# Kernel optimization log

Hardware: AMD Instinct MI355X
Metric: run time of the kernel (lower is better)

The kernel has to match this reference:

```python
import math
import jax, jax.numpy as jnp
import numpy as np

IN_D = 16
H_DIM = 256
NB_STEPS = 50
B = 8192


def _cc_weights(nb_steps):
    # Clenshaw-Curtis quadrature weights and nodes, exactly as the torch code.
    k = np.arange(0, nb_steps + 1, dtype=np.float64).reshape(-1, 1)
    lam = np.cos(k @ k.T * math.pi / nb_steps)
    lam[:, 0] = 0.5
    lam[:, -1] = 0.5 * lam[:, -1]
    lam = lam * 2.0 / nb_steps
    W = np.arange(0, nb_steps + 1, dtype=np.float64).reshape(-1, 1)
    W[1::2] = 0.0
    W = 2.0 / (1.0 - W ** 2)
    W[0] = 1.0
    W[1::2] = 0.0
    cc = (lam.T @ W).astype(np.float32)  # [nb_steps+1, 1]
    steps = np.cos(np.arange(0, nb_steps + 1) * math.pi / nb_steps).astype(np.float32)  # [nb_steps+1]
    return jnp.asarray(cc), jnp.asarray(steps)


def setup_inputs() -> dict:
    key = jax.random.key(0)
    ks = jax.random.split(key, 16)
    s = 0.05
    return {
        "x": jax.random.normal(ks[0], (B, 1), jnp.float32),
        "h": jax.random.normal(ks[1], (B, IN_D - 1), jnp.float32),
        "iw1": jax.random.normal(ks[2], (H_DIM, IN_D), jnp.float32) * s,
        "ib1": jax.random.normal(ks[3], (H_DIM,), jnp.float32) * s,
        "iw2": jax.random.normal(ks[4], (H_DIM, H_DIM), jnp.float32) * s,
        "ib2": jax.random.normal(ks[5], (H_DIM,), jnp.float32) * s,
        "iw3": jax.random.normal(ks[6], (1, H_DIM), jnp.float32) * s,
        "ib3": jax.random.normal(ks[7], (1,), jnp.float32) * s,
        "nw1": jax.random.normal(ks[8], (H_DIM, IN_D - 1), jnp.float32) * s,
        "nb1": jax.random.normal(ks[9], (H_DIM,), jnp.float32) * s,
        "nw2": jax.random.normal(ks[10], (H_DIM, H_DIM), jnp.float32) * s,
        "nb2": jax.random.normal(ks[11], (H_DIM,), jnp.float32) * s,
        "nw3": jax.random.normal(ks[12], (2, H_DIM), jnp.float32) * s,
        "nb3": jax.random.normal(ks[13], (2,), jnp.float32) * s,
        "nb_steps": NB_STEPS,
    }


def _integrand(z, iw1, ib1, iw2, ib2, iw3, ib3):
    # IntegrandNN: Linear-ReLU-Linear-ReLU-Linear-ELU, then +1.0
    a = jax.nn.relu(z @ iw1.T + ib1)
    a = jax.nn.relu(a @ iw2.T + ib2)
    return jax.nn.elu(a @ iw3.T + ib3) + 1.0


def reference(x, h, iw1, ib1, iw2, ib2, iw3, ib3, nw1, nb1, nw2, nb2, nw3, nb3, nb_steps):
    cc, steps = _cc_weights(int(nb_steps))  # cc: [N+1,1], steps: [N+1]
    Bn, n_pts = x.shape[0], int(nb_steps) + 1
    # x0 = 0, so quadrature nodes X_k = x * (steps_k + 1) / 2 -> [B, N+1, 1]
    X = x[:, None, :] * ((steps[None, :, None] + 1.0) * 0.5)
    Xf = X.reshape(-1, 1)                                             # [B*(N+1), 1]
    Hf = jnp.broadcast_to(h[:, None, :], (Bn, n_pts, h.shape[1])).reshape(-1, h.shape[1])
    z = jnp.concatenate([Xf, Hf], axis=1)                             # [B*(N+1), in_d]
    f = _integrand(z, iw1, ib1, iw2, ib2, iw3, ib3).reshape(Bn, n_pts, 1)
    integral = jnp.sum(f * cc[None, :, :], axis=1) * x * 0.5          # [B, 1]
    # conditioner net on h: Linear-ReLU-Linear-ReLU-Linear -> [B, 2]
    a = jax.nn.relu(h @ nw1.T + nb1)
    a = jax.nn.relu(a @ nw2.T + nb2)
    out = a @ nw3.T + nb3
    offset = out[:, :1]
    scaling = jnp.exp(out[:, 1:2])
    return scaling * integral + offset
```

## Files before the change

### kernel.cpp

```cpp
#include <hip/hip_runtime.h>
#include <hip/hip_bf16.h>
#include <math.h>

#define BATCH 8192
#define HD    256
#define NPTS  51
#define MTOT  (BATCH*NPTS)

typedef __bf16 bf16x8 __attribute__((ext_vector_type(8)));
typedef float  f32x4  __attribute__((ext_vector_type(4)));

#define OFF_IW2P  0
#define OFF_W1X   131072
#define OFF_CC    132096
#define OFF_STEPS 132352
#define OFF_OFFS  132608
#define OFF_SCAL  165376
#define OFF_G1    198144
#define OFF_FV0   8586752
#define OFF_FV1   10257920

__device__ __forceinline__ unsigned short f2bf(float f) {
    union { float f; unsigned u; } v; v.f = f;
    unsigned r = v.u + 0x7FFFu + ((v.u >> 16) & 1u);
    return (unsigned short)(r >> 16);
}

__device__ __forceinline__ unsigned pk2bf(float lo, float hi) {
    __hip_bfloat162 t = __float22bfloat162_rn(float2{lo, hi});
    union { __hip_bfloat162 b; unsigned u; } v; v.b = t;
    return v.u;
}

__global__ void k1_fused(const float* __restrict__ iw2, const float* __restrict__ nw1,
                         const float* __restrict__ iw1, const float* __restrict__ ib1,
                         const float* __restrict__ nb1, const float* __restrict__ h,
                         const float* __restrict__ nw2, const float* __restrict__ nb2,
                         const float* __restrict__ nw3, const float* __restrict__ nb3,
                         unsigned short* iw2p, float* w1xs, float* cc, float* steps,
                         float* __restrict__ g1, float* __restrict__ offs,
                         float* __restrict__ scal) {
    int blk = blockIdx.x, tid = threadIdx.x;
    if (blk < 256) {
        int t = blk * 256 + tid;
        int n = t >> 8, k = t & 255;
        int half = n >> 7, nl = n & 127, c = k >> 3, j = k & 7;
        iw2p[half * 32768 + c * 1024 + nl * 8 + j] = f2bf(iw2[t]);
    } else if (blk == 256) {
        w1xs[tid] = iw1[tid * 16];
        const float PI_F = 3.14159265358979323846f;
        if (tid <= 50) {
            int j = tid;
            float s = 0.f;
            for (int i = 0; i <= 50; i += 2) {
                float w = (i == 0) ? 1.f : 2.f / (1.f - (float)(i * i));
                float l;
                if (j == 0 || j == 50) l = 0.5f;
                else { int r = (i * j) % 100; l = __cosf((float)r * (PI_F / 50.f)); }
                s += l * w;
            }
            cc[j]    = s * (2.f / 50.f);
            steps[j] = __cosf((float)j * (PI_F / 50.f));
        }
    } else {
        __shared__ float hs[16][15];
        __shared__ unsigned short a1s[16][264];
        __shared__ float Pp[4 * 2 * 16];
        int b0 = (blk - 257) * 16, n = tid;
        if (tid < 240) { int bb = tid / 15, j = tid % 15; hs[bb][j] = h[(b0 + bb) * 15 + j]; }
        __syncthreads();
        float ir[16], nr[15];
        const float4* ip = (const float4*)(iw1 + n * 16);
        ((float4*)ir)[0] = ip[0]; ((float4*)ir)[1] = ip[1];
        ((float4*)ir)[2] = ip[2]; ((float4*)ir)[3] = ip[3];
        #pragma unroll
        for (int j = 0; j < 15; ++j) nr[j] = nw1[n * 15 + j];
        float bi = ib1[n], bn = nb1[n];
        #pragma unroll
        for (int bb = 0; bb < 16; ++bb) {
            float g = bi, a = bn;
            #pragma unroll
            for (int j = 0; j < 15; ++j) { float hv = hs[bb][j]; g += hv * ir[j + 1]; a += hv * nr[j]; }
            g1[(b0 + bb) * 256 + n] = g;
            a1s[bb][n] = f2bf(fmaxf(a, 0.f));
        }
        __syncthreads();

        int lane = tid & 63, w = tid >> 6, l16 = lane & 15, quad = lane >> 4;
        f32x4 acc[4];
        #pragma unroll
        for (int nt = 0; nt < 4; ++nt) acc[nt] = (f32x4){0.f, 0.f, 0.f, 0.f};
        #pragma unroll
        for (int ks = 0; ks < 8; ++ks) {
            bf16x8 af = *(const bf16x8*)&a1s[l16][ks * 32 + quad * 8];
            #pragma unroll
            for (int nt = 0; nt < 4; ++nt) {
                const float* np = nw2 + (w * 64 + nt * 16 + l16) * 256 + ks * 32 + quad * 8;
                float4 f0 = ((const float4*)np)[0];
                float4 f1 = ((const float4*)np)[1];
                union { uint4 u; bf16x8 v; } bf;
                bf.u.x = pk2bf(f0.x, f0.y); bf.u.y = pk2bf(f0.z, f0.w);
                bf.u.z = pk2bf(f1.x, f1.y); bf.u.w = pk2bf(f1.z, f1.w);
                acc[nt] = __builtin_amdgcn_mfma_f32_16x16x32_bf16(af, bf.v, acc[nt], 0, 0, 0);
            }
        }
        float p0[4], p1[4];
        #pragma unroll
        for (int i = 0; i < 4; ++i) { p0[i] = 0.f; p1[i] = 0.f; }
        #pragma unroll
        for (int nt = 0; nt < 4; ++nt) {
            int nn = w * 64 + nt * 16 + l16;
            float bias = nb2[nn], wa = nw3[nn], wb = nw3[256 + nn];
            #pragma unroll
            for (int i = 0; i < 4; ++i) {
                float v = acc[nt][i] + bias;
                v = v > 0.f ? v : 0.f;
                p0[i] += v * wa;
                p1[i] += v * wb;
            }
        }
        #pragma unroll
        for (int mask = 1; mask < 16; mask <<= 1)
            #pragma unroll
            for (int i = 0; i < 4; ++i) {
                p0[i] += __shfl_xor(p0[i], mask, 64);
                p1[i] += __shfl_xor(p1[i], mask, 64);
            }
        if (l16 == 0) {
            #pragma unroll
            for (int i = 0; i < 4; ++i) {
                int r = quad * 4 + i;
                Pp[w * 32 + r]      = p0[i];
                Pp[w * 32 + 16 + r] = p1[i];
            }
        }
        __syncthreads();
        if (tid < 16) {
            float s0 = Pp[tid]      + Pp[32 + tid] + Pp[64 + tid] + Pp[96 + tid]  + nb3[0];
            float s1 = Pp[16 + tid] + Pp[48 + tid] + Pp[80 + tid] + Pp[112 + tid] + nb3[1];
            offs[b0 + tid] = s0;
            scal[b0 + tid] = __expf(s1);
        }
    }
}

__launch_bounds__(256, 4)
__global__ void k2_main(const float* __restrict__ x, const float* __restrict__ g1,
                        const float* __restrict__ w1xs, const unsigned short* __restrict__ iw2p,
                        const float* __restrict__ ib2, const float* __restrict__ iw3,
                        const float* __restrict__ steps,
                        float* __restrict__ fv0, float* __restrict__ fv1) {
    __shared__ __align__(16) unsigned char smem[37888];
    float* Pp = (float*)smem;

    int tid = threadIdx.x;
    int bid = blockIdx.x;
    int hf  = bid & 1;
    int m0  = (bid >> 1) * 128;
    int lane = tid & 63, w = tid >> 6;
    int l16 = lane & 15, quad = lane >> 4;

    unsigned blo = (unsigned)(((unsigned long long)(unsigned)m0 * 657931ull) >> 25);

    const unsigned char* bsrc = (const unsigned char*)iw2p + hf * 65536 + tid * 16;

    #pragma unroll
    for (int it = 0; it < 4; ++it)
        __builtin_amdgcn_global_load_lds(
            (const __attribute__((address_space(1))) unsigned int*)(bsrc + it * 4096),
            (__attribute__((address_space(3))) unsigned int*)(smem + tid * 16 + it * 4096),
            16, 0, 0);
    __builtin_amdgcn_global_load_lds(
        (const __attribute__((address_space(1))) unsigned int*)((const unsigned char*)(g1 + blo * 256) + tid * 16),
        (__attribute__((address_space(3))) unsigned int*)(smem + 32768 + tid * 16),
        16, 0, 0);
    if (w == 0)
        __builtin_amdgcn_global_load_lds(
            (const __attribute__((address_space(1))) unsigned int*)((const unsigned char*)w1xs + lane * 16),
            (__attribute__((address_space(3))) unsigned int*)(smem + 36864 + lane * 16),
            16, 0, 0);

    float xs_[2]; int rel_[2];
    #pragma unroll
    for (int mt = 0; mt < 2; ++mt) {
        int m = m0 + w * 32 + mt * 16 + l16;
        unsigned b = (unsigned)(((unsigned long long)(unsigned)m * 657931ull) >> 25);
        int p = m - (int)b * 51;
        xs_[mt] = x[b] * (steps[p] + 1.f) * 0.5f;
        rel_[mt] = (int)(b - blo) * 256;
    }

    f32x4 acc[2][8];
    #pragma unroll
    for (int mt = 0; mt < 2; ++mt)
        #pragma unroll
        for (int nt = 0; nt < 8; ++nt)
            acc[mt][nt] = (f32x4){0.f, 0.f, 0.f, 0.f};

    const float* Ag = (const float*)(smem + 32768);
    const float* Wl = (const float*)(smem + 36864);

    #pragma unroll
    for (int kc = 0; kc < 4; ++kc) {
        __syncthreads();
        if (kc < 3) {
            const unsigned char* s2 = bsrc + (kc + 1) * 16384;
            unsigned char* d2 = smem + ((kc + 1) & 1) * 16384 + tid * 16;
            #pragma unroll
            for (int it = 0; it < 4; ++it)
                __builtin_amdgcn_global_load_lds(
                    (const __attribute__((address_space(1))) unsigned int*)(s2 + it * 4096),
                    (__attribute__((address_space(3))) unsigned int*)(d2 + it * 4096),
                    16, 0, 0);
        }
        const unsigned short* Bl = (const unsigned short*)(smem + (kc & 1) * 16384);
        #pragma unroll
        for (int s = 0; s < 2; ++s) {
            int ks = kc * 2 + s;
            int ko = ks * 32 + quad * 8;
            int cl = s * 4 + quad;

            union { uint4 u; bf16x8 v; } af[2];
            {
                float4 w0 = ((const float4*)(Wl + ko))[0];
                float4 w1 = ((const float4*)(Wl + ko))[1];
                #pragma unroll
                for (int mt = 0; mt < 2; ++mt) {
                    const float* gp = Ag + rel_[mt] + ko;
                    float4 ga  = ((const float4*)gp)[0];
                    float4 gb2 = ((const float4*)gp)[1];
                    float xs = xs_[mt];
                    float a0 = fmaxf(ga.x  + xs * w0.x, 0.f);
                    float a1 = fmaxf(ga.y  + xs * w0.y, 0.f);
                    float a2 = fmaxf(ga.z  + xs * w0.z, 0.f);
                    float a3 = fmaxf(ga.w  + xs * w0.w, 0.f);
                    float a4 = fmaxf(gb2.x + xs * w1.x, 0.f);
                    float a5 = fmaxf(gb2.y + xs * w1.y, 0.f);
                    float a6 = fmaxf(gb2.z + xs * w1.z, 0.f);
                    float a7 = fmaxf(gb2.w + xs * w1.w, 0.f);
                    af[mt].u.x = pk2bf(a0, a1); af[mt].u.y = pk2bf(a2, a3);
                    af[mt].u.z = pk2bf(a4, a5); af[mt].u.w = pk2bf(a6, a7);
                }
            }

            #pragma unroll
            for (int g = 0; g < 2; ++g) {
                bf16x8 bfr[4];
                #pragma unroll
                for (int nt = 0; nt < 4; ++nt)
                    bfr[nt] = *(const bf16x8*)(Bl + (cl * 128 + (g * 4 + nt) * 16 + l16) * 8);
                #pragma unroll
                for (int mt = 0; mt < 2; ++mt)
                    #pragma unroll
                    for (int nt = 0; nt < 4; ++nt)
                        acc[mt][g * 4 + nt] = __builtin_amdgcn_mfma_f32_16x16x32_bf16(
                            af[mt].v, bfr[nt], acc[mt][g * 4 + nt], 0, 0, 0);
            }
        }
    }

    float pf[2][4];
    #pragma unroll
    for (int mt = 0; mt < 2; ++mt)
        #pragma unroll
        for (int i = 0; i < 4; ++i) pf[mt][i] = 0.f;
    #pragma unroll
    for (int nt = 0; nt < 8; ++nt) {
        int n = hf * 128 + nt * 16 + l16;
        float bias = ib2[n], w3 = iw3[n];
        #pragma unroll
        for (int mt = 0; mt < 2; ++mt)
            #pragma unroll
            for (int i = 0; i < 4; ++i) {
                float v = acc[mt][nt][i] + bias;
                v = v > 0.f ? v : 0.f;
                pf[mt][i] += v * w3;
            }
    }
    __syncthreads();
    #pragma unroll
    for (int mt = 0; mt < 2; ++mt)
        #pragma unroll
        for (int i = 0; i < 4; ++i) {
            int row = w * 32 + mt * 16 + quad * 4 + i;
            Pp[row * 20 + l16] = pf[mt][i];
        }
    __syncthreads();
    if (tid < 128) {
        const float4* pp = (const float4*)(Pp + tid * 20);
        float4 v0 = pp[0], v1 = pp[1], v2 = pp[2], v3 = pp[3];
        float s = v0.x + v0.y + v0.z + v0.w + v1.x + v1.y + v1.z + v1.w
                + v2.x + v2.y + v2.z + v2.w + v3.x + v3.y + v3.z + v3.w;
        (hf ? fv1 : fv0)[m0 + tid] = s;
    }
}

__global__ void k4_final(const float* __restrict__ x, const float* __restrict__ fv0,
                         const float* __restrict__ fv1, const float* __restrict__ ib3,
                         const float* __restrict__ cc,
                         const float* __restrict__ offs, const float* __restrict__ scal,
                         float* __restrict__ out) {
    int tid = threadIdx.x;
    int wv = tid >> 6, lane = tid & 63;
    int b = blockIdx.x * 4 + wv;
    float v = 0.f;
    if (lane < 51) {
        int m = b * 51 + lane;
        float s = fv0[m] + fv1[m] + ib3[0];
        float f = s > 0.f ? s + 1.f : __expf(s);
        v = f * cc[lane];
    }
    #pragma unroll
    for (int mask = 1; mask < 64; mask <<= 1) v += __shfl_xor(v, mask, 64);
    if (lane == 0)
        out[b] = scal[b] * (0.5f * x[b] * v) + offs[b];
}

extern "C" void kernel_launch(void* const* d_in, const int* in_sizes, int n_in,
                              void* d_out, int out_size, void* d_ws, size_t ws_size,
                              hipStream_t stream) {
    const float* x   = (const float*)d_in[0];
    const float* h   = (const float*)d_in[1];
    const float* iw1 = (const float*)d_in[2];
    const float* ib1 = (const float*)d_in[3];
    const float* iw2 = (const float*)d_in[4];
    const float* ib2 = (const float*)d_in[5];
    const float* iw3 = (const float*)d_in[6];
    const float* ib3 = (const float*)d_in[7];
    const float* nw1 = (const float*)d_in[8];
    const float* nb1 = (const float*)d_in[9];
    const float* nw2 = (const float*)d_in[10];
    const float* nb2 = (const float*)d_in[11];
    const float* nw3 = (const float*)d_in[12];
    const float* nb3 = (const float*)d_in[13];
    float* out = (float*)d_out;

    char* ws = (char*)d_ws;
    unsigned short* iw2p = (unsigned short*)(ws + OFF_IW2P);
    float* w1xs  = (float*)(ws + OFF_W1X);
    float* cc    = (float*)(ws + OFF_CC);
    float* steps = (float*)(ws + OFF_STEPS);
    float* offs  = (float*)(ws + OFF_OFFS);
    float* scal  = (float*)(ws + OFF_SCAL);
    float* g1    = (float*)(ws + OFF_G1);
    float* fv0   = (float*)(ws + OFF_FV0);
    float* fv1   = (float*)(ws + OFF_FV1);

    k1_fused<<<dim3(769), dim3(256), 0, stream>>>(iw2, nw1, iw1, ib1, nb1, h,
                                                  nw2, nb2, nw3, nb3,
                                                  iw2p, w1xs, cc, steps, g1, offs, scal);
    k2_main<<<dim3((MTOT / 128) * 2), dim3(256), 0, stream>>>(x, g1, w1xs, iw2p, ib2, iw3,
                                                              steps, fv0, fv1);
    k4_final<<<dim3(BATCH / 4), dim3(256), 0, stream>>>(x, fv0, fv1, ib3, cc, offs, scal, out);
}
```

Measured before the change: 162.8 us.

## Compute full N=256 per block in k2, fuse ELU and CC weighting into epilogue

Each k2 block now covers all 256 output columns instead of splitting N across two blocks. This halves the block count and removes the duplicated first-layer activation computation and the second partial-sum buffer. The layer-1 precompute g1 and the w1x weights are read straight from global memory instead of staged in LDS, and ELU plus the quadrature-weight multiply move into the k2 epilogue so k4 only reduces. In exchange the accumulator doubles to 32 MFMA tiles and LDS grows to 64KB, which lowers the occupancy bound from 4 to 2 blocks per CU.

```diff
diff --git a/kernel.cpp b/kernel.cpp
--- a/kernel.cpp
+++ b/kernel.cpp
@@ -3,7 +3,6 @@
 #include <math.h>
 
 #define BATCH 8192
-#define HD    256
 #define NPTS  51
 #define MTOT  (BATCH*NPTS)
 
@@ -17,8 +16,7 @@
 #define OFF_OFFS  132608
 #define OFF_SCAL  165376
 #define OFF_G1    198144
-#define OFF_FV0   8586752
-#define OFF_FV1   10257920
+#define OFF_FVALS 8586752
 
 __device__ __forceinline__ unsigned short f2bf(float f) {
     union { float f; unsigned u; } v; v.f = f;
@@ -144,40 +142,29 @@
     }
 }
 
-__launch_bounds__(256, 4)
+__launch_bounds__(256, 2)
 __global__ void k2_main(const float* __restrict__ x, const float* __restrict__ g1,
                         const float* __restrict__ w1xs, const unsigned short* __restrict__ iw2p,
                         const float* __restrict__ ib2, const float* __restrict__ iw3,
-                        const float* __restrict__ steps,
-                        float* __restrict__ fv0, float* __restrict__ fv1) {
-    __shared__ __align__(16) unsigned char smem[37888];
+                        const float* __restrict__ ib3, const float* __restrict__ cc,
+                        const float* __restrict__ steps, float* __restrict__ fvals) {
+    __shared__ __align__(16) unsigned char smem[65536];
     float* Pp = (float*)smem;
 
     int tid = threadIdx.x;
-    int bid = blockIdx.x;
-    int hf  = bid & 1;
-    int m0  = (bid >> 1) * 128;
+    int m0  = blockIdx.x * 128;
     int lane = tid & 63, w = tid >> 6;
     int l16 = lane & 15, quad = lane >> 4;
 
-    unsigned blo = (unsigned)(((unsigned long long)(unsigned)m0 * 657931ull) >> 25);
-
-    const unsigned char* bsrc = (const unsigned char*)iw2p + hf * 65536 + tid * 16;
-
-    #pragma unroll
-    for (int it = 0; it < 4; ++it)
+    int hh = tid >> 7, t7 = tid & 127;
+    const unsigned char* bsrc = (const unsigned char*)iw2p + hh * 65536 + t7 * 16;
+    unsigned char* bds0 = smem + hh * 16384 + t7 * 16;
+
+    #pragma unroll
+    for (int it = 0; it < 8; ++it)
         __builtin_amdgcn_global_load_lds(
-            (const __attribute__((address_space(1))) unsigned int*)(bsrc + it * 4096),
-            (__attribute__((address_space(3))) unsigned int*)(smem + tid * 16 + it * 4096),
-            16, 0, 0);
-    __builtin_amdgcn_global_load_lds(
-        (const __attribute__((address_space(1))) unsigned int*)((const unsigned char*)(g1 + blo * 256) + tid * 16),
-        (__attribute__((address_space(3))) unsigned int*)(smem + 32768 + tid * 16),
-        16, 0, 0);
-    if (w == 0)
-        __builtin_amdgcn_global_load_lds(
-            (const __attribute__((address_space(1))) unsigned int*)((const unsigned char*)w1xs + lane * 16),
-            (__attribute__((address_space(3))) unsigned int*)(smem + 36864 + lane * 16),
+            (const __attribute__((address_space(1))) unsigned int*)(bsrc + it * 2048),
+            (__attribute__((address_space(3))) unsigned int*)(bds0 + it * 2048),
             16, 0, 0);
 
     float xs_[2]; int rel_[2];
@@ -187,68 +174,66 @@
         unsigned b = (unsigned)(((unsigned long long)(unsigned)m * 657931ull) >> 25);
         int p = m - (int)b * 51;
         xs_[mt] = x[b] * (steps[p] + 1.f) * 0.5f;
-        rel_[mt] = (int)(b - blo) * 256;
-    }
-
-    f32x4 acc[2][8];
+        rel_[mt] = (int)b * 256;
+    }
+
+    f32x4 acc[2][16];
     #pragma unroll
     for (int mt = 0; mt < 2; ++mt)
         #pragma unroll
-        for (int nt = 0; nt < 8; ++nt)
+        for (int nt = 0; nt < 16; ++nt)
             acc[mt][nt] = (f32x4){0.f, 0.f, 0.f, 0.f};
-
-    const float* Ag = (const float*)(smem + 32768);
-    const float* Wl = (const float*)(smem + 36864);
 
     #pragma unroll
     for (int kc = 0; kc < 4; ++kc) {
         __syncthreads();
         if (kc < 3) {
             const unsigned char* s2 = bsrc + (kc + 1) * 16384;
-            unsigned char* d2 = smem + ((kc + 1) & 1) * 16384 + tid * 16;
-            #pragma unroll
-            for (int it = 0; it < 4; ++it)
+            unsigned char* d2 = smem + ((kc + 1) & 1) * 32768 + hh * 16384 + t7 * 16;
+            #pragma unroll
+            for (int it = 0; it < 8; ++it)
                 __builtin_amdgcn_global_load_lds(
-                    (const __attribute__((address_space(1))) unsigned int*)(s2 + it * 4096),
-                    (__attribute__((address_space(3))) unsigned int*)(d2 + it * 4096),
+                    (const __attribute__((address_space(1))) unsigned int*)(s2 + it * 2048),
+                    (__attribute__((address_space(3))) unsigned int*)(d2 + it * 2048),
                     16, 0, 0);
         }
-        const unsigned short* Bl = (const unsigned short*)(smem + (kc & 1) * 16384);
+        const unsigned short* Bl = (const unsigned short*)(smem + (kc & 1) * 32768);
         #pragma unroll
         for (int s = 0; s < 2; ++s) {
-            int ks = kc * 2 + s;
-            int ko = ks * 32 + quad * 8;
+            int ko = kc * 64 + s * 32 + quad * 8;
             int cl = s * 4 + quad;
 
+            float4 w0 = ((const float4*)(w1xs + ko))[0];
+            float4 w1 = ((const float4*)(w1xs + ko))[1];
+
             union { uint4 u; bf16x8 v; } af[2];
-            {
-                float4 w0 = ((const float4*)(Wl + ko))[0];
-                float4 w1 = ((const float4*)(Wl + ko))[1];
-                #pragma unroll
-                for (int mt = 0; mt < 2; ++mt) {
-                    const float* gp = Ag + rel_[mt] + ko;
-                    float4 ga  = ((const float4*)gp)[0];
-                    float4 gb2 = ((const float4*)gp)[1];
-                    float xs = xs_[mt];
-                    float a0 = fmaxf(ga.x  + xs * w0.x, 0.f);
-                    float a1 = fmaxf(ga.y  + xs * w0.y, 0.f);
-                    float a2 = fmaxf(ga.z  + xs * w0.z, 0.f);
-                    float a3 = fmaxf(ga.w  + xs * w0.w, 0.f);
-                    float a4 = fmaxf(gb2.x + xs * w1.x, 0.f);
-                    float a5 = fmaxf(gb2.y + xs * w1.y, 0.f);
-                    float a6 = fmaxf(gb2.z + xs * w1.z, 0.f);
-                    float a7 = fmaxf(gb2.w + xs * w1.w, 0.f);
-                    af[mt].u.x = pk2bf(a0, a1); af[mt].u.y = pk2bf(a2, a3);
-                    af[mt].u.z = pk2bf(a4, a5); af[mt].u.w = pk2bf(a6, a7);
-                }
-            }
-
-            #pragma unroll
-            for (int g = 0; g < 2; ++g) {
+            #pragma unroll
+            for (int mt = 0; mt < 2; ++mt) {
+                const float* gp = g1 + rel_[mt] + ko;
+                float4 ga  = ((const float4*)gp)[0];
+                float4 gb2 = ((const float4*)gp)[1];
+                float xs = xs_[mt];
+                float a0 = fmaxf(fmaf(xs, w0.x, ga.x),  0.f);
+                float a1 = fmaxf(fmaf(xs, w0.y, ga.y),  0.f);
+                float a2 = fmaxf(fmaf(xs, w0.z, ga.z),  0.f);
+                float a3 = fmaxf(fmaf(xs, w0.w, ga.w),  0.f);
+                float a4 = fmaxf(fmaf(xs, w1.x, gb2.x), 0.f);
+                float a5 = fmaxf(fmaf(xs, w1.y, gb2.y), 0.f);
+                float a6 = fmaxf(fmaf(xs, w1.z, gb2.z), 0.f);
+                float a7 = fmaxf(fmaf(xs, w1.w, gb2.w), 0.f);
+                af[mt].u.x = pk2bf(a0, a1); af[mt].u.y = pk2bf(a2, a3);
+                af[mt].u.z = pk2bf(a4, a5); af[mt].u.w = pk2bf(a6, a7);
+            }
+
+            #pragma unroll
+            for (int g = 0; g < 4; ++g) {
                 bf16x8 bfr[4];
                 #pragma unroll
-                for (int nt = 0; nt < 4; ++nt)
-                    bfr[nt] = *(const bf16x8*)(Bl + (cl * 128 + (g * 4 + nt) * 16 + l16) * 8);
+                for (int nt = 0; nt < 4; ++nt) {
+                    int n = (g * 4 + nt) * 16 + l16;
+                    int h2 = n >> 7, nl = n & 127;
+                    bfr[nt] = *(const bf16x8*)(Bl + h2 * 8192 + cl * 1024 + nl * 8);
+                }
                 #pragma unroll
                 for (int mt = 0; mt < 2; ++mt)
                     #pragma unroll
@@ -265,14 +250,14 @@
         #pragma unroll
         for (int i = 0; i < 4; ++i) pf[mt][i] = 0.f;
     #pragma unroll
-    for (int nt = 0; nt < 8; ++nt) {
-        int n = hf * 128 + nt * 16 + l16;
+    for (int j = 0; j < 16; ++j) {
+        int n = j * 16 + l16;
         float bias = ib2[n], w3 = iw3[n];
         #pragma unroll
         for (int mt = 0; mt < 2; ++mt)
             #pragma unroll
             for (int i = 0; i < 4; ++i) {
-                float v = acc[mt][nt][i] + bias;
+                float v = acc[mt][j][i] + bias;
                 v = v > 0.f ? v : 0.f;
                 pf[mt][i] += v * w3;
             }
@@ -291,25 +276,22 @@
         float4 v0 = pp[0], v1 = pp[1], v2 = pp[2], v3 = pp[3];
         float s = v0.x + v0.y + v0.z + v0.w + v1.x + v1.y + v1.z + v1.w
                 + v2.x + v2.y + v2.z + v2.w + v3.x + v3.y + v3.z + v3.w;
-        (hf ? fv1 : fv0)[m0 + tid] = s;
-    }
-}
-
-__global__ void k4_final(const float* __restrict__ x, const float* __restrict__ fv0,
-                         const float* __restrict__ fv1, const float* __restrict__ ib3,
-                         const float* __restrict__ cc,
+        s += ib3[0];
+        int m = m0 + tid;
+        unsigned b = (unsigned)(((unsigned long long)(unsigned)m * 657931ull) >> 25);
+        int p = m - (int)b * 51;
+        float f = s > 0.f ? s + 1.f : __expf(s);
+        fvals[m] = f * cc[p];
+    }
+}
+
+__global__ void k4_final(const float* __restrict__ x, const float* __restrict__ fvals,
                          const float* __restrict__ offs, const float* __restrict__ scal,
                          float* __restrict__ out) {
     int tid = threadIdx.x;
     int wv = tid >> 6, lane = tid & 63;
     int b = blockIdx.x * 4 + wv;
-    float v = 0.f;
-    if (lane < 51) {
-        int m = b * 51 + lane;
-        float s = fv0[m] + fv1[m] + ib3[0];
-        float f = s > 0.f ? s + 1.f : __expf(s);
-        v = f * cc[lane];
-    }
+    float v = (lane < 51) ? fvals[b * 51 + lane] : 0.f;
     #pragma unroll
     for (int mask = 1; mask < 64; mask <<= 1) v += __shfl_xor(v, mask, 64);
     if (lane == 0)
@@ -343,13 +325,12 @@
     float* offs  = (float*)(ws + OFF_OFFS);
     float* scal  = (float*)(ws + OFF_SCAL);
     float* g1    = (float*)(ws + OFF_G1);
-    float* fv0   = (float*)(ws + OFF_FV0);
-    float* fv1   = (float*)(ws + OFF_FV1);
+    float* fvals = (float*)(ws + OFF_FVALS);
 
     k1_fused<<<dim3(769), dim3(256), 0, stream>>>(iw2, nw1, iw1, ib1, nb1, h,
                                                   nw2, nb2, nw3, nb3,
                                                   iw2p, w1xs, cc, steps, g1, offs, scal);
-    k2_main<<<dim3((MTOT / 128) * 2), dim3(256), 0, stream>>>(x, g1, w1xs, iw2p, ib2, iw3,
-                                                              steps, fv0, fv1);
-    k4_final<<<dim3(BATCH / 4), dim3(256), 0, stream>>>(x, fv0, fv1, ib3, cc, offs, scal, out);
-}
+    k2_main<<<dim3(MTOT / 128), dim3(256), 0, stream>>>(x, g1, w1xs, iw2p, ib2, iw3,
+                                                        ib3, cc, steps, fvals);
+    k4_final<<<dim3(BATCH / 4), dim3(256), 0, stream>>>(x, fvals, offs, scal, out);
+}
```

New measurement: 179.6 us. +10.3%, slower.
